# Performance work log

Measured on AMD Instinct MI355X. Metric: run time of the kernel, lower is better.

## Reference

```python
import jax, jax.numpy as jnp
import numpy as np

B, L, C = 8, 4096, 512
WS, SHIFT, H = 64, 32, 16
HD = C // H
HID = 4 * C


def _ln(x, w, b):
    m = x.mean(-1, keepdims=True)
    v = ((x - m) ** 2).mean(-1, keepdims=True)
    return (x - m) / jnp.sqrt(v + 1e-5) * w + b


def _attn_mask():
    # 0 / -100 mask for shifted windows, shape (nW, WS, WS)
    img = np.zeros((L,), np.float32)
    cnt = 0
    for s in (slice(0, L - WS), slice(L - WS, L - SHIFT), slice(L - SHIFT, L)):
        img[s] = cnt
        cnt += 1
    mw = img.reshape(L // WS, WS)
    d = mw[:, :, None] - mw[:, None, :]
    return jnp.asarray(np.where(d != 0, -100.0, 0.0).astype(np.float32))


def _cpb_coords():
    # log-spaced continuous relative coords, shape (2*WS-1, 1)
    r = np.arange(-(WS - 1), WS, dtype=np.float32) / (WS - 1) * 8.0
    t = np.sign(r) * np.log2(np.abs(r) + 1.0) / np.log2(8.0)
    return jnp.asarray(t[:, None].astype(np.float32))


def _rel_index():
    c = np.arange(WS)
    return jnp.asarray((c[:, None] - c[None, :] + WS - 1).astype(np.int32))


def setup_inputs():
    key = jax.random.key(0)
    ks = jax.random.split(key, 8)
    n = jax.random.normal
    return {
        "x": n(ks[0], (B, L, C), jnp.float32),
        "qkv_w": n(ks[1], (3 * C, C), jnp.float32) * 0.02,
        "q_bias": jnp.zeros((C,), jnp.float32),
        "v_bias": jnp.zeros((C,), jnp.float32),
        "logit_scale": jnp.log(10.0 * jnp.ones((H, 1, 1), jnp.float32)),
        "cpb_w1": n(ks[2], (512, 1), jnp.float32) * 0.02,
        "cpb_b1": jnp.zeros((512,), jnp.float32),
        "cpb_w2": n(ks[3], (H, 512), jnp.float32) * 0.02,
        "proj_w": n(ks[4], (C, C), jnp.float32) * 0.02,
        "proj_b": jnp.zeros((C,), jnp.float32),
        "norm1_w": jnp.ones((C,), jnp.float32),
        "norm1_b": jnp.zeros((C,), jnp.float32),
        "norm2_w": jnp.ones((C,), jnp.float32),
        "norm2_b": jnp.zeros((C,), jnp.float32),
        "fc1_w": n(ks[5], (HID, C), jnp.float32) * 0.02,
        "fc1_b": jnp.zeros((HID,), jnp.float32),
        "fc2_w": n(ks[6], (C, HID), jnp.float32) * 0.02,
        "fc2_b": jnp.zeros((C,), jnp.float32),
    }


def reference(x, qkv_w, q_bias, v_bias, logit_scale, cpb_w1, cpb_b1, cpb_w2,
              proj_w, proj_b, norm1_w, norm1_b, norm2_w, norm2_b,
              fc1_w, fc1_b, fc2_w, fc2_b):
    nW = L // WS
    shortcut = x
    # cyclic shift + window partition
    xs = jnp.roll(x, -SHIFT, axis=1)
    xw = xs.reshape(B * nW, WS, C)
    # qkv with q/v bias only (k bias is zero)
    qkv_b = jnp.concatenate([q_bias, jnp.zeros_like(v_bias), v_bias])
    qkv = (xw @ qkv_w.T + qkv_b).reshape(B * nW, WS, 3, H, HD)
    qkv = qkv.transpose(2, 0, 3, 1, 4)  # (3, B*nW, H, WS, HD)
    q, k, v = qkv[0], qkv[1], qkv[2]
    # cosine attention with learned, clamped per-head temperature
    qn = q / jnp.maximum(jnp.linalg.norm(q, axis=-1, keepdims=True), 1e-12)
    kn = k / jnp.maximum(jnp.linalg.norm(k, axis=-1, keepdims=True), 1e-12)
    attn = jnp.einsum('whnd,whmd->whnm', qn, kn)
    scale = jnp.exp(jnp.minimum(logit_scale, jnp.log(100.0)))  # (H,1,1)
    attn = attn * scale
    # continuous relative position bias via small MLP
    tbl = jax.nn.relu(_cpb_coords() @ cpb_w1.T + cpb_b1) @ cpb_w2.T  # (2WS-1, H)
    bias = tbl[_rel_index()]  # (WS, WS, H)
    bias = 16.0 * jax.nn.sigmoid(bias.transpose(2, 0, 1))  # (H, WS, WS)
    attn = attn + bias[None]
    # shift mask (0 / -100), per window
    mask = _attn_mask()  # (nW, WS, WS)
    attn = attn.reshape(B, nW, H, WS, WS) + mask[None, :, None]
    attn = jax.nn.softmax(attn.reshape(B * nW, H, WS, WS), axis=-1)
    out = jnp.einsum('whnm,whmd->whnd', attn, v)
    out = out.transpose(0, 2, 1, 3).reshape(B * nW, WS, C)
    out = out @ proj_w.T + proj_b
    # window reverse + reverse shift
    out = jnp.roll(out.reshape(B, L, C), SHIFT, axis=1)
    # Swin v2 post-norm residuals
    x1 = shortcut + _ln(out, norm1_w, norm1_b)
    h = jax.nn.gelu(x1 @ fc1_w.T + fc1_b, approximate=False) @ fc2_w.T + fc2_b
    return x1 + _ln(h, norm2_w, norm2_b)
```

## Files before the change

kernel.cpp:

```cpp
#include <hip/hip_runtime.h>
#include <hip/hip_bf16.h>
#include <math.h>

typedef unsigned short u16;
typedef __bf16 bf16x8 __attribute__((ext_vector_type(8)));
typedef float f32x4 __attribute__((ext_vector_type(4)));
typedef unsigned short u16x8 __attribute__((ext_vector_type(8)));
typedef unsigned short u16x4 __attribute__((ext_vector_type(4)));
typedef unsigned short u16x2 __attribute__((ext_vector_type(2)));

#define DEV static __device__ __forceinline__

DEV float b2f(u16 v) { unsigned u = ((unsigned)v) << 16; return __builtin_bit_cast(float, u); }
DEV u16 f2bf(float f) {
  unsigned u = __builtin_bit_cast(unsigned, f);
  u += 0x7fffu + ((u >> 16) & 1u);
  return (u16)(u >> 16);
}

DEV void async16(const void* g, void* l) {
  __builtin_amdgcn_global_load_lds(
      (const __attribute__((address_space(1))) void*)g,
      (__attribute__((address_space(3))) void*)l, 16, 0, 0);
}

__global__ __launch_bounds__(256) void cvt_all_kernel(
    const float* __restrict__ x,  const float* __restrict__ wq,
    const float* __restrict__ wp, const float* __restrict__ w1,
    const float* __restrict__ w2,
    u16* __restrict__ dx, u16* __restrict__ dq, u16* __restrict__ dp,
    u16* __restrict__ d1, u16* __restrict__ d2)
{
  const int i = blockIdx.x * 256 + threadIdx.x;
  const float* s; u16* d; int off;
  if (i < 4194304)      { s = x;  d = dx; off = i; }
  else if (i < 4390912) { s = wq; d = dq; off = i - 4194304; }
  else if (i < 4456448) { s = wp; d = dp; off = i - 4390912; }
  else if (i < 4718592) { s = w1; d = d1; off = i - 4456448; }
  else if (i < 4980736) { s = w2; d = d2; off = i - 4718592; }
  else return;
  float4 v = ((const float4*)s)[off];
  u16x4 o;
  o[0] = f2bf(v.x); o[1] = f2bf(v.y); o[2] = f2bf(v.z); o[3] = f2bf(v.w);
  ((u16x4*)d)[off] = o;
}

__global__ __launch_bounds__(64) void cpb1_kernel(
    const float* __restrict__ w1, const float* __restrict__ b1,
    const float* __restrict__ w2, float* __restrict__ tbl)
{
  const int r = blockIdx.x, h = blockIdx.y;
  const int lane = threadIdx.x;
  float rv = (float)(r - 63) * (8.0f / 63.0f);
  float sgn = (rv > 0.f) ? 1.f : ((rv < 0.f) ? -1.f : 0.f);
  float t = sgn * log2f(fabsf(rv) + 1.f) * (1.f / 3.f);
  float part = 0.f;
  for (int k = lane; k < 512; k += 64) {
    float hid = fmaxf(t * w1[k] + b1[k], 0.f);
    part += hid * w2[h * 512 + k];
  }
  #pragma unroll
  for (int o = 32; o > 0; o >>= 1) part += __shfl_down(part, o);
  if (lane == 0) tbl[r * 16 + h] = part;
}

__global__ __launch_bounds__(256) void cpb2_kernel(
    const float* __restrict__ tbl, float* __restrict__ btbl)
{
  const int h = blockIdx.x;
  for (int idx = threadIdx.x; idx < 4096; idx += 256) {
    int i = idx >> 6, j = idx & 63;
    float v = tbl[(i - j + 63) * 16 + h];
    btbl[h * 4096 + idx] = 16.f / (1.f + __expf(-v));
  }
}

__global__ __launch_bounds__(256, 4) void gemm_qkv(
    const u16* __restrict__ A, const u16* __restrict__ W,
    const float* __restrict__ bias1, const float* __restrict__ bias2,
    u16* __restrict__ out, int nby, int N, int K)
{
  __shared__ __attribute__((aligned(16))) u16 lA[4096];
  __shared__ __attribute__((aligned(16))) u16 lB[4096];
  const int tid = threadIdx.x;
  const int lane = tid & 63;
  const int wv = tid >> 6;
  const int q8 = (int)gridDim.x >> 3;
  const int swb = (blockIdx.x & 7) * q8 + (blockIdx.x >> 3);
  const int m0 = (swb / nby) * 128;
  const int n0 = (swb % nby) * 128;
  const int wm = (wv >> 1) * 64;
  const int wn = (wv & 1) * 64;
  const int fr = lane & 15;
  const int hi = lane >> 4;
  const int sr = tid >> 2;
  const int sp = tid & 3;
  f32x4 acc[4][4] = {};

  for (int k0 = 0; k0 < K; k0 += 32) {
    #pragma unroll
    for (int i = 0; i < 2; ++i) {
      const int r = i * 64 + sr;
      const int kk = k0 + ((sp ^ ((r >> 1) & 3)) << 3);
      const int mg = m0 + r;
      const int bb = mg >> 12;
      const int p = mg & 4095;
      const long ga = ((long)bb << 12) + ((p + 32) & 4095);
      async16(A + ga * (long)K + kk, lA + r * 32 + sp * 8);
      async16(W + (size_t)(n0 + r) * K + kk, lB + r * 32 + sp * 8);
    }
    __syncthreads();
    bf16x8 fa[4], fb[4];
    #pragma unroll
    for (int t = 0; t < 4; ++t) {
      const int ra = wm + t * 16 + fr;
      fa[t] = *(const bf16x8*)&lA[ra * 32 + ((hi ^ ((ra >> 1) & 3)) << 3)];
      const int rb = wn + t * 16 + fr;
      fb[t] = *(const bf16x8*)&lB[rb * 32 + ((hi ^ ((rb >> 1) & 3)) << 3)];
    }
    #pragma unroll
    for (int mi = 0; mi < 4; ++mi)
      #pragma unroll
      for (int ni = 0; ni < 4; ++ni)
        acc[mi][ni] = __builtin_amdgcn_mfma_f32_16x16x32_bf16(fa[mi], fb[ni], acc[mi][ni], 0, 0, 0);
    __syncthreads();
  }

  const int lrow = hi * 4;
  #pragma unroll
  for (int mi = 0; mi < 4; ++mi) {
    #pragma unroll
    for (int ni = 0; ni < 4; ++ni) {
      const int n = n0 + wn + ni * 16 + fr;
      const int which = n >> 9, c = n & 511;
      const int hh = c >> 5, d = c & 31;
      const float bias = (which == 0) ? bias1[c] : (which == 2 ? bias2[c] : 0.f);
      #pragma unroll
      for (int r = 0; r < 4; ++r) {
        const int m = m0 + wm + mi * 16 + lrow + r;
        const int g = m >> 6, ii = m & 63;
        out[(size_t)which * 16777216 + (size_t)g * 32768 + hh * 2048 + ii * 32 + d] =
            f2bf(acc[mi][ni][r] + bias);
      }
    }
  }
}

template <int MODE>
__global__ __launch_bounds__(512, 2) void gemm_bt(
    const u16* __restrict__ A, const u16* __restrict__ W,
    const float* __restrict__ bias1, const float* __restrict__ bias2,
    u16* __restrict__ out, int nby, int N, int K)
{
  extern __shared__ __attribute__((aligned(16))) u16 smem[];
  const int tid = threadIdx.x;
  const int lane = tid & 63;
  const int wv = tid >> 6;
  const int q8 = (int)gridDim.x >> 3;
  const int swb = (blockIdx.x & 7) * q8 + (blockIdx.x >> 3);
  const int m0 = (swb / nby) * 256;
  const int n0 = (swb % nby) * 256;
  const int wm = (wv >> 2) * 128;
  const int wn = (wv & 3) * 64;
  const int fr = lane & 15;
  const int hi = lane >> 4;
  const int srow = tid >> 3;
  const int kb = (tid & 7) ^ (srow & 7);
  f32x4 acc[8][4] = {};

  auto stageA = [&](int buf, int k0, int i) {
    const int r = srow + (i << 6);
    const u16* src;
    if constexpr (MODE == 1) {
      const int kk = k0 + kb * 8;
      src = A + (size_t)(kk >> 5) * 1048576 + (size_t)(m0 + r) * 32 + (kk & 31);
    } else {
      src = A + (size_t)(m0 + r) * K + k0 + kb * 8;
    }
    async16(src, smem + buf * 16384 + ((i << 9) + tid) * 8);
  };
  auto stageB = [&](int buf, int k0, int i) {
    const int r = srow + (i << 6);
    async16(W + (size_t)(n0 + r) * K + k0 + kb * 8,
            smem + 32768 + buf * 16384 + ((i << 9) + tid) * 8);
  };
  auto stage_part = [&](int buf, int k0, int part) {
    if (part == 0)      { stageB(buf, k0, 0); stageB(buf, k0, 1); }
    else if (part == 1) { stageB(buf, k0, 2); stageB(buf, k0, 3); }
    else if (part == 2) { stageA(buf, k0, 0); stageA(buf, k0, 2); }
    else                { stageA(buf, k0, 1); stageA(buf, k0, 3); }
  };

  auto phase_compute = [&](const u16* lac, const u16* lbc, int mh, int ks) {
    bf16x8 fa[4], fb[4];
    const int sw = hi + (ks << 2);
    #pragma unroll
    for (int mi = 0; mi < 4; ++mi) {
      const int r = wm + ((mh << 2) + mi) * 16 + fr;
      fa[mi] = *(const bf16x8*)&lac[r * 64 + ((sw ^ (r & 7)) << 3)];
    }
    #pragma unroll
    for (int ni = 0; ni < 4; ++ni) {
      const int r = wn + ni * 16 + fr;
      fb[ni] = *(const bf16x8*)&lbc[r * 64 + ((sw ^ (r & 7)) << 3)];
    }
    asm volatile("s_waitcnt lgkmcnt(0)" ::: "memory");
    __builtin_amdgcn_sched_barrier(0);
    __builtin_amdgcn_s_setprio(1);
    #pragma unroll
    for (int mi = 0; mi < 4; ++mi)
      #pragma unroll
      for (int ni = 0; ni < 4; ++ni)
        acc[(mh << 2) + mi][ni] = __builtin_amdgcn_mfma_f32_16x16x32_bf16(
            fa[mi], fb[ni], acc[(mh << 2) + mi][ni], 0, 0, 0);
    __builtin_amdgcn_s_setprio(0);
  };

  const int NT = K >> 6;
  stage_part(0, 0, 0); stage_part(0, 0, 1); stage_part(0, 0, 2); stage_part(0, 0, 3);
  int cur = 0;
  for (int kt = 0; kt < NT; ++kt) {
    const bool hn = (kt + 1) < NT;
    const int nk0 = (kt + 1) << 6;
    const u16* lac = smem + cur * 16384;
    const u16* lbc = smem + 32768 + cur * 16384;
    const int nb = cur ^ 1;
    asm volatile("s_waitcnt vmcnt(2)" ::: "memory");
    __builtin_amdgcn_s_barrier();
    if (hn) stage_part(nb, nk0, 0);
    phase_compute(lac, lbc, 0, 0);
    if (hn) { asm volatile("s_waitcnt vmcnt(2)" ::: "memory"); }
    else    { asm volatile("s_waitcnt vmcnt(0)" ::: "memory"); }
    __builtin_amdgcn_s_barrier();
    if (hn) stage_part(nb, nk0, 1);
    phase_compute(lac, lbc, 1, 0);
    if (hn) stage_part(nb, nk0, 2);
    phase_compute(lac, lbc, 0, 1);
    if (hn) stage_part(nb, nk0, 3);
    phase_compute(lac, lbc, 1, 1);
    cur ^= 1;
  }

  const int lrow = hi * 4;
  #pragma unroll
  for (int mi = 0; mi < 8; ++mi) {
    #pragma unroll
    for (int ni = 0; ni < 4; ++ni) {
      const int n = n0 + wn + ni * 16 + fr;
      #pragma unroll
      for (int r = 0; r < 4; ++r) {
        const int m = m0 + wm + mi * 16 + lrow + r;
        float v = acc[mi][ni][r];
        if constexpr (MODE == 2) {
          float t = v + bias1[n];
          float u = t * t;
          float z = t * (1.5957691216f + 0.0713548163f * u);
          float ge = t / (1.f + __expf(-z));
          out[(size_t)m * N + n] = f2bf(ge);
        } else {
          out[(size_t)m * N + n] = f2bf(v + bias1[n]);
        }
      }
    }
  }
}

__global__ __launch_bounds__(256) void gemm_sm3(
    const u16* __restrict__ A, const u16* __restrict__ W,
    const float* __restrict__ bias1,
    u16* __restrict__ out, int nby, int N, int K)
{
  __shared__ __attribute__((aligned(16))) u16 lA[2][8192];
  __shared__ __attribute__((aligned(16))) u16 lB[2][8192];
  const int tid = threadIdx.x;
  const int wid = tid >> 6;
  const int lane = tid & 63;
  const int q8 = (int)gridDim.x >> 3;
  const int swb = (blockIdx.x & 7) * q8 + (blockIdx.x >> 3);
  const int m0 = (swb / nby) * 128;
  const int n0 = (swb % nby) * 128;
  const int wm = (wid >> 1) * 64;
  const int wn = (wid & 1) * 64;
  f32x4 acc[4][4] = {};

  const int srow8 = lane >> 3;
  const int kel = ((lane & 7) ^ srow8) * 8;

  auto stage = [&](int b, int k0) {
    #pragma unroll
    for (int cc = 0; cc < 4; ++cc) {
      const int rb = wid * 32 + cc * 8;
      const int r = rb + srow8;
      async16(A + (size_t)(m0 + r) * K + k0 + kel, &lA[b][rb * 64]);
      async16(W + (size_t)(n0 + r) * K + k0 + kel, &lB[b][rb * 64]);
    }
  };

  const int NT = K >> 6;
  stage(0, 0);
  __syncthreads();
  int cur = 0;
  const int fr = lane & 15;
  const int hi = lane >> 4;
  const int fsw = fr & 7;
  for (int kt = 0; kt < NT; ++kt) {
    if (kt + 1 < NT) stage(cur ^ 1, (kt + 1) << 6);
    #pragma unroll
    for (int ks = 0; ks < 2; ++ks) {
      bf16x8 fa[4], fb[4];
      #pragma unroll
      for (int t = 0; t < 4; ++t) {
        const int ra = wm + t * 16 + fr;
        fa[t] = *(const bf16x8*)&lA[cur][ra * 64 + (((hi + 4 * ks) ^ fsw) << 3)];
        const int rbq = wn + t * 16 + fr;
        fb[t] = *(const bf16x8*)&lB[cur][rbq * 64 + (((hi + 4 * ks) ^ fsw) << 3)];
      }
      #pragma unroll
      for (int mi = 0; mi < 4; ++mi)
        #pragma unroll
        for (int ni = 0; ni < 4; ++ni)
          acc[mi][ni] = __builtin_amdgcn_mfma_f32_16x16x32_bf16(fa[mi], fb[ni], acc[mi][ni], 0, 0, 0);
    }
    __syncthreads();
    cur ^= 1;
  }

  const int lrow = (lane >> 4) * 4;
  #pragma unroll
  for (int mi = 0; mi < 4; ++mi)
    #pragma unroll
    for (int ni = 0; ni < 4; ++ni) {
      const int n = n0 + wn + ni * 16 + fr;
      #pragma unroll
      for (int r = 0; r < 4; ++r) {
        const int m = m0 + wm + mi * 16 + lrow + r;
        out[(size_t)m * N + n] = f2bf(acc[mi][ni][r] + bias1[n]);
      }
    }
}

__global__ __launch_bounds__(256) void attn_kernel(
    const u16* __restrict__ qkv, const float* __restrict__ ls,
    const float* __restrict__ btbl, u16* __restrict__ attnT)
{
  const int gg = blockIdx.x;
  const int w = threadIdx.x >> 6;
  const int lane = threadIdx.x & 63;
  __shared__ __attribute__((aligned(16))) u16 vt[4][2048];
  __shared__ __attribute__((aligned(16))) u16 pl[4][4096];
  const bool maskw = ((gg & 63) == 63);
  const int fr = lane & 15;
  const int fkq = (lane >> 4) * 8;
  const int crow = (lane >> 4) * 4;

  for (int t = 0; t < 4; ++t) {
    const int h = w * 4 + t;
    const size_t bgh = (size_t)gg * 32768 + (size_t)h * 2048;

    {
      const u16x8* vp = (const u16x8*)(qkv + 33554432 + bgh + (size_t)lane * 32);
      #pragma unroll
      for (int c = 0; c < 4; ++c) {
        u16x8 vr = vp[c];
        #pragma unroll
        for (int e = 0; e < 8; ++e) {
          const int d = c * 8 + e;
          const int addr = d * 64 + (((lane >> 3) ^ (d & 7)) << 3) + (lane & 7);
          vt[w][addr] = vr[e];
        }
      }
    }

    const float scale = __expf(fminf(ls[h], 4.6051701859880914f));
    bf16x8 qa[4], kb[4];
    #pragma unroll
    for (int mi = 0; mi < 4; ++mi) {
      u16x8 raw = *(const u16x8*)(qkv + bgh + (size_t)(mi * 16 + fr) * 32 + fkq);
      float f[8]; float ssum = 0.f;
      #pragma unroll
      for (int e = 0; e < 8; ++e) { f[e] = b2f(raw[e]); ssum += f[e] * f[e]; }
      ssum += __shfl_xor(ssum, 16); ssum += __shfl_xor(ssum, 32);
      const float mul = scale / fmaxf(sqrtf(ssum), 1e-12f);
      u16x8 tmp;
      #pragma unroll
      for (int e = 0; e < 8; ++e) tmp[e] = f2bf(f[e] * mul);
      qa[mi] = __builtin_bit_cast(bf16x8, tmp);
    }
    #pragma unroll
    for (int ni = 0; ni < 4; ++ni) {
      u16x8 raw = *(const u16x8*)(qkv + 16777216 + bgh + (size_t)(ni * 16 + fr) * 32 + fkq);
      float f[8]; float ssum = 0.f;
      #pragma unroll
      for (int e = 0; e < 8; ++e) { f[e] = b2f(raw[e]); ssum += f[e] * f[e]; }
      ssum += __shfl_xor(ssum, 16); ssum += __shfl_xor(ssum, 32);
      const float mul = 1.f / fmaxf(sqrtf(ssum), 1e-12f);
      u16x8 tmp;
      #pragma unroll
      for (int e = 0; e < 8; ++e) tmp[e] = f2bf(f[e] * mul);
      kb[ni] = __builtin_bit_cast(bf16x8, tmp);
    }

    f32x4 s[4][4] = {};
    __builtin_amdgcn_s_setprio(1);
    #pragma unroll
    for (int mi = 0; mi < 4; ++mi)
      #pragma unroll
      for (int ni = 0; ni < 4; ++ni)
        s[mi][ni] = __builtin_amdgcn_mfma_f32_16x16x32_bf16(qa[mi], kb[ni], s[mi][ni], 0, 0, 0);
    __builtin_amdgcn_s_setprio(0);

    const float mh = scale + 16.f;
    float inv_[4][4];
    #pragma unroll
    for (int mi = 0; mi < 4; ++mi) {
      #pragma unroll
      for (int r = 0; r < 4; ++r) {
        const int row = mi * 16 + crow + r;
        float es = 0.f;
        #pragma unroll
        for (int ni = 0; ni < 4; ++ni) {
          const int col = ni * 16 + fr;
          float sv = s[mi][ni][r] + btbl[h * 4096 + row * 64 + col];
          if (maskw && ((row < 32) != (col < 32))) sv -= 100.f;
          const float e = __expf(sv - mh);
          s[mi][ni][r] = e;
          es += e;
        }
        es += __shfl_xor(es, 1); es += __shfl_xor(es, 2);
        es += __shfl_xor(es, 4); es += __shfl_xor(es, 8);
        inv_[mi][r] = 1.f / fmaxf(es, 1e-37f);
      }
    }

    #pragma unroll
    for (int mi = 0; mi < 4; ++mi)
      #pragma unroll
      for (int r = 0; r < 4; ++r) {
        const int row = mi * 16 + crow + r;
        #pragma unroll
        for (int ni = 0; ni < 4; ++ni) {
          const int col = ni * 16 + fr;
          const int addr = row * 64 + (((col >> 3) ^ (row & 7)) << 3) + (col & 7);
          pl[w][addr] = f2bf(s[mi][ni][r]);
        }
      }

    f32x4 o[4][2] = {};
    #pragma unroll
    for (int ks = 0; ks < 2; ++ks) {
      bf16x8 vbf[2];
      #pragma unroll
      for (int np = 0; np < 2; ++np) {
        const int d = np * 16 + fr;
        const int jb = (lane >> 4) + ks * 4;
        vbf[np] = *(const bf16x8*)&vt[w][d * 64 + ((jb ^ (d & 7)) << 3)];
      }
      __builtin_amdgcn_s_setprio(1);
      #pragma unroll
      for (int mp = 0; mp < 4; ++mp) {
        const int row = mp * 16 + fr;
        const int cb = (lane >> 4) + ks * 4;
        bf16x8 paf = *(const bf16x8*)&pl[w][row * 64 + ((cb ^ (row & 7)) << 3)];
        o[mp][0] = __builtin_amdgcn_mfma_f32_16x16x32_bf16(paf, vbf[0], o[mp][0], 0, 0, 0);
        o[mp][1] = __builtin_amdgcn_mfma_f32_16x16x32_bf16(paf, vbf[1], o[mp][1], 0, 0, 0);
      }
      __builtin_amdgcn_s_setprio(0);
    }

    #pragma unroll
    for (int mp = 0; mp < 4; ++mp)
      #pragma unroll
      for (int r = 0; r < 4; ++r) {
        const int row = mp * 16 + crow + r;
        const float iv = inv_[mp][r];
        u16* op = attnT + (size_t)h * 1048576 + (size_t)(gg * 64 + row) * 32;
        op[fr]      = f2bf(o[mp][0][r] * iv);
        op[16 + fr] = f2bf(o[mp][1][r] * iv);
      }
  }
}

__global__ __launch_bounds__(256) void ln1_kernel(
    const u16* __restrict__ proj, const float* __restrict__ x,
    const float* __restrict__ w, const float* __restrict__ bb,
    u16* __restrict__ x1h)
{
  const int row = blockIdx.x * 4 + (threadIdx.x >> 6);
  const int lane = threadIdx.x & 63;
  const int b = row >> 12, l = row & 4095;
  const int p = (l - 32) & 4095;
  const size_t srow = (((size_t)b << 12) + p) << 9;
  const int c0 = lane * 8;
  u16x8 pv = *(const u16x8*)(proj + srow + c0);
  float v[8]; float s = 0.f, ss = 0.f;
  #pragma unroll
  for (int e = 0; e < 8; ++e) { v[e] = b2f(pv[e]); s += v[e]; ss += v[e] * v[e]; }
  #pragma unroll
  for (int o = 32; o > 0; o >>= 1) { s += __shfl_xor(s, o); ss += __shfl_xor(ss, o); }
  const float mean = s * (1.f / 512.f);
  const float var = ss * (1.f / 512.f) - mean * mean;
  const float rstd = rsqrtf(var + 1e-5f);
  const size_t orow = (size_t)row << 9;
  float4 x0 = *(const float4*)(x + orow + c0);
  float4 x1 = *(const float4*)(x + orow + c0 + 4);
  const float xs[8] = {x0.x, x0.y, x0.z, x0.w, x1.x, x1.y, x1.z, x1.w};
  u16x8 ho;
  #pragma unroll
  for (int e = 0; e < 8; ++e)
    ho[e] = f2bf(xs[e] + (v[e] - mean) * rstd * w[c0 + e] + bb[c0 + e]);
  *(u16x8*)(x1h + orow + c0) = ho;
}

__global__ __launch_bounds__(256) void ln2_kernel(
    const u16* __restrict__ fc2, const u16* __restrict__ x1h,
    const float* __restrict__ w, const float* __restrict__ bb,
    float* __restrict__ out)
{
  const int row = blockIdx.x * 4 + (threadIdx.x >> 6);
  const int lane = threadIdx.x & 63;
  const size_t r512 = (size_t)row << 9;
  const int c0 = lane * 8;
  u16x8 pv = *(const u16x8*)(fc2 + r512 + c0);
  float v[8]; float s = 0.f, ss = 0.f;
  #pragma unroll
  for (int e = 0; e < 8; ++e) { v[e] = b2f(pv[e]); s += v[e]; ss += v[e] * v[e]; }
  #pragma unroll
  for (int o = 32; o > 0; o >>= 1) { s += __shfl_xor(s, o); ss += __shfl_xor(ss, o); }
  const float mean = s * (1.f / 512.f);
  const float var = ss * (1.f / 512.f) - mean * mean;
  const float rstd = rsqrtf(var + 1e-5f);
  u16x8 xv = *(const u16x8*)(x1h + r512 + c0);
  float r[8];
  #pragma unroll
  for (int e = 0; e < 8; ++e)
    r[e] = b2f(xv[e]) + (v[e] - mean) * rstd * w[c0 + e] + bb[c0 + e];
  float4 o0, o1;
  o0.x = r[0]; o0.y = r[1]; o0.z = r[2]; o0.w = r[3];
  o1.x = r[4]; o1.y = r[5]; o1.z = r[6]; o1.w = r[7];
  *(float4*)(out + r512 + c0) = o0;
  *(float4*)(out + r512 + c0 + 4) = o1;
}

extern "C" void kernel_launch(void* const* d_in, const int* in_sizes, int n_in,
                              void* d_out, int out_size, void* d_ws, size_t ws_size,
                              hipStream_t stream) {
  const float* x        = (const float*)d_in[0];
  const float* qkv_w    = (const float*)d_in[1];
  const float* q_bias   = (const float*)d_in[2];
  const float* v_bias   = (const float*)d_in[3];
  const float* lscale   = (const float*)d_in[4];
  const float* cpb_w1   = (const float*)d_in[5];
  const float* cpb_b1   = (const float*)d_in[6];
  const float* cpb_w2   = (const float*)d_in[7];
  const float* proj_w   = (const float*)d_in[8];
  const float* proj_b   = (const float*)d_in[9];
  const float* n1w      = (const float*)d_in[10];
  const float* n1b      = (const float*)d_in[11];
  const float* n2w      = (const float*)d_in[12];
  const float* n2b      = (const float*)d_in[13];
  const float* fc1_w    = (const float*)d_in[14];
  const float* fc1_b    = (const float*)d_in[15];
  const float* fc2_w    = (const float*)d_in[16];
  const float* fc2_b    = (const float*)d_in[17];

  if (ws_size < 134217728u) return;
  char* ws = (char*)d_ws;
  u16* wqkv   = (u16*)(ws + 0);
  u16* wproj  = (u16*)(ws + 1572864);
  u16* wfc1   = (u16*)(ws + 2097152);
  u16* wfc2   = (u16*)(ws + 4194304);
  float* btbl = (float*)(ws + 6291456);
  u16* qkv    = (u16*)(ws + 6553600);
  u16* projo  = (u16*)(ws + 6553600);
  u16* hbuf   = (u16*)(ws + 6553600);
  u16* fc2oh  = (u16*)(ws + 73662464);
  u16* x1h    = (u16*)(ws + 94371840);
  float* tbl  = (float*)(ws + 127926272);
  u16* xbf   = (u16*)d_out;
  u16* attnT = (u16*)d_out;
  float* out = (float*)d_out;

  hipFuncSetAttribute((const void*)gemm_bt<1>, hipFuncAttributeMaxDynamicSharedMemorySize, 131072);
  hipFuncSetAttribute((const void*)gemm_bt<2>, hipFuncAttributeMaxDynamicSharedMemorySize, 131072);

  cvt_all_kernel<<<19456, 256, 0, stream>>>(
      x, qkv_w, proj_w, fc1_w, fc2_w, xbf, wqkv, wproj, wfc1, wfc2);
  cpb1_kernel<<<dim3(127, 16), 64, 0, stream>>>(cpb_w1, cpb_b1, cpb_w2, tbl);
  cpb2_kernel<<<16, 256, 0, stream>>>(tbl, btbl);

  gemm_qkv<<<3072, 256, 0, stream>>>(
      xbf, wqkv, q_bias, v_bias, qkv, 12, 1536, 512);
  attn_kernel<<<512, 256, 0, stream>>>(qkv, lscale, btbl, attnT);
  gemm_bt<1><<<256, 512, 131072, stream>>>(
      attnT, wproj, proj_b, nullptr, projo, 2, 512, 512);
  ln1_kernel<<<8192, 256, 0, stream>>>(projo, x, n1w, n1b, x1h);
  for (int half = 0; half < 2; ++half) {
    const u16* a2 = x1h + (size_t)half * 8388608;
    gemm_bt<2><<<512, 512, 131072, stream>>>(
        a2, wfc1, fc1_b, nullptr, hbuf, 8, 2048, 512);
    gemm_sm3<<<512, 256, 0, stream>>>(
        hbuf, wfc2, fc2_b, fc2oh, 4, 512, 2048);
    ln2_kernel<<<4096, 256, 0, stream>>>(
        fc2oh, a2, n2w, n2b, out + (size_t)half * 8388608);
  }
}
```

Before: 400.9 us.

## Double-buffer QKV GEMM loads and replace projection GEMM with 128x128 kernel

Result: slower. 425.2 us (+6.1%).

```diff
diff --git a/kernel.cpp b/kernel.cpp
--- a/kernel.cpp
+++ b/kernel.cpp
@@ -80,8 +80,8 @@
     const float* __restrict__ bias1, const float* __restrict__ bias2,
     u16* __restrict__ out, int nby, int N, int K)
 {
-  __shared__ __attribute__((aligned(16))) u16 lA[4096];
-  __shared__ __attribute__((aligned(16))) u16 lB[4096];
+  __shared__ __attribute__((aligned(16))) u16 lA[2][4096];
+  __shared__ __attribute__((aligned(16))) u16 lB[2][4096];
   const int tid = threadIdx.x;
   const int lane = tid & 63;
   const int wv = tid >> 6;
@@ -97,7 +97,7 @@
   const int sp = tid & 3;
   f32x4 acc[4][4] = {};
 
-  for (int k0 = 0; k0 < K; k0 += 32) {
+  auto stage = [&](int b, int k0) {
     #pragma unroll
     for (int i = 0; i < 2; ++i) {
       const int r = i * 64 + sr;
@@ -106,17 +106,24 @@
       const int bb = mg >> 12;
       const int p = mg & 4095;
       const long ga = ((long)bb << 12) + ((p + 32) & 4095);
-      async16(A + ga * (long)K + kk, lA + r * 32 + sp * 8);
-      async16(W + (size_t)(n0 + r) * K + kk, lB + r * 32 + sp * 8);
-    }
-    __syncthreads();
+      async16(A + ga * (long)K + kk, &lA[b][r * 32 + sp * 8]);
+      async16(W + (size_t)(n0 + r) * K + kk, &lB[b][r * 32 + sp * 8]);
+    }
+  };
+
+  const int NT = K >> 5;
+  stage(0, 0);
+  __syncthreads();
+  int cur = 0;
+  for (int kt = 0; kt < NT; ++kt) {
+    if (kt + 1 < NT) stage(cur ^ 1, (kt + 1) << 5);
     bf16x8 fa[4], fb[4];
     #pragma unroll
     for (int t = 0; t < 4; ++t) {
       const int ra = wm + t * 16 + fr;
-      fa[t] = *(const bf16x8*)&lA[ra * 32 + ((hi ^ ((ra >> 1) & 3)) << 3)];
+      fa[t] = *(const bf16x8*)&lA[cur][ra * 32 + ((hi ^ ((ra >> 1) & 3)) << 3)];
       const int rb = wn + t * 16 + fr;
-      fb[t] = *(const bf16x8*)&lB[rb * 32 + ((hi ^ ((rb >> 1) & 3)) << 3)];
+      fb[t] = *(const bf16x8*)&lB[cur][rb * 32 + ((hi ^ ((rb >> 1) & 3)) << 3)];
     }
     #pragma unroll
     for (int mi = 0; mi < 4; ++mi)
@@ -124,6 +131,7 @@
       for (int ni = 0; ni < 4; ++ni)
         acc[mi][ni] = __builtin_amdgcn_mfma_f32_16x16x32_bf16(fa[mi], fb[ni], acc[mi][ni], 0, 0, 0);
     __syncthreads();
+    cur ^= 1;
   }
 
   const int lrow = hi * 4;
@@ -144,6 +152,82 @@
       }
     }
   }
+}
+
+__global__ __launch_bounds__(256) void gemm_proj(
+    const u16* __restrict__ A, const u16* __restrict__ W,
+    const float* __restrict__ bias1,
+    u16* __restrict__ out, int nby, int N, int K)
+{
+  __shared__ __attribute__((aligned(16))) u16 lA[2][8192];
+  __shared__ __attribute__((aligned(16))) u16 lB[2][8192];
+  const int tid = threadIdx.x;
+  const int wid = tid >> 6;
+  const int lane = tid & 63;
+  const int q8 = (int)gridDim.x >> 3;
+  const int swb = (blockIdx.x & 7) * q8 + (blockIdx.x >> 3);
+  const int m0 = (swb / nby) * 128;
+  const int n0 = (swb % nby) * 128;
+  const int wm = (wid >> 1) * 64;
+  const int wn = (wid & 1) * 64;
+  f32x4 acc[4][4] = {};
+
+  const int srow8 = lane >> 3;
+  const int kel = ((lane & 7) ^ srow8) * 8;
+
+  auto stage = [&](int b, int k0) {
+    #pragma unroll
+    for (int cc = 0; cc < 4; ++cc) {
+      const int rb = wid * 32 + cc * 8;
+      const int r = rb + srow8;
+      const int kk = k0 + kel;
+      async16(A + (size_t)(kk >> 5) * 1048576 + (size_t)(m0 + r) * 32 + (kk & 31),
+              &lA[b][rb * 64]);
+      async16(W + (size_t)(n0 + r) * K + kk, &lB[b][rb * 64]);
+    }
+  };
+
+  const int NT = K >> 6;
+  stage(0, 0);
+  __syncthreads();
+  int cur = 0;
+  const int fr = lane & 15;
+  const int hi = lane >> 4;
+  const int fsw = fr & 7;
+  for (int kt = 0; kt < NT; ++kt) {
+    if (kt + 1 < NT) stage(cur ^ 1, (kt + 1) << 6);
+    #pragma unroll
+    for (int ks = 0; ks < 2; ++ks) {
+      bf16x8 fa[4], fb[4];
+      #pragma unroll
+      for (int t = 0; t < 4; ++t) {
+        const int ra = wm + t * 16 + fr;
+        fa[t] = *(const bf16x8*)&lA[cur][ra * 64 + (((hi + 4 * ks) ^ fsw) << 3)];
+        const int rbq = wn + t * 16 + fr;
+        fb[t] = *(const bf16x8*)&lB[cur][rbq * 64 + (((hi + 4 * ks) ^ fsw) << 3)];
+      }
+      #pragma unroll
+      for (int mi = 0; mi < 4; ++mi)
+        #pragma unroll
+        for (int ni = 0; ni < 4; ++ni)
+          acc[mi][ni] = __builtin_amdgcn_mfma_f32_16x16x32_bf16(fa[mi], fb[ni], acc[mi][ni], 0, 0, 0);
+    }
+    __syncthreads();
+    cur ^= 1;
+  }
+
+  const int lrow = (lane >> 4) * 4;
+  #pragma unroll
+  for (int mi = 0; mi < 4; ++mi)
+    #pragma unroll
+    for (int ni = 0; ni < 4; ++ni) {
+      const int n = n0 + wn + ni * 16 + fr;
+      #pragma unroll
+      for (int r = 0; r < 4; ++r) {
+        const int m = m0 + wm + mi * 16 + lrow + r;
+        out[(size_t)m * N + n] = f2bf(acc[mi][ni][r] + bias1[n]);
+      }
+    }
 }
 
 template <int MODE>
@@ -170,14 +254,8 @@
 
   auto stageA = [&](int buf, int k0, int i) {
     const int r = srow + (i << 6);
-    const u16* src;
-    if constexpr (MODE == 1) {
-      const int kk = k0 + kb * 8;
-      src = A + (size_t)(kk >> 5) * 1048576 + (size_t)(m0 + r) * 32 + (kk & 31);
-    } else {
-      src = A + (size_t)(m0 + r) * K + k0 + kb * 8;
-    }
-    async16(src, smem + buf * 16384 + ((i << 9) + tid) * 8);
+    async16(A + (size_t)(m0 + r) * K + k0 + kb * 8,
+            smem + buf * 16384 + ((i << 9) + tid) * 8);
   };
   auto stageB = [&](int buf, int k0, int i) {
     const int r = srow + (i << 6);
@@ -580,7 +658,6 @@
   u16* attnT = (u16*)d_out;
   float* out = (float*)d_out;
 
-  hipFuncSetAttribute((const void*)gemm_bt<1>, hipFuncAttributeMaxDynamicSharedMemorySize, 131072);
   hipFuncSetAttribute((const void*)gemm_bt<2>, hipFuncAttributeMaxDynamicSharedMemorySize, 131072);
 
   cvt_all_kernel<<<19456, 256, 0, stream>>>(
@@ -591,8 +668,8 @@
   gemm_qkv<<<3072, 256, 0, stream>>>(
       xbf, wqkv, q_bias, v_bias, qkv, 12, 1536, 512);
   attn_kernel<<<512, 256, 0, stream>>>(qkv, lscale, btbl, attnT);
-  gemm_bt<1><<<256, 512, 131072, stream>>>(
-      attnT, wproj, proj_b, nullptr, projo, 2, 512, 512);
+  gemm_proj<<<1024, 256, 0, stream>>>(
+      attnT, wproj, proj_b, projo, 4, 512, 512);
   ln1_kernel<<<8192, 256, 0, stream>>>(projo, x, n1w, n1b, x1h);
   for (int half = 0; half < 2; ++half) {
     const u16* a2 = x1h + (size_t)half * 8388608;
```
